# Performance work log

Hardware: AMD Instinct MI355X
Metric: run time of the kernel (lower is better)

The kernel has to match this reference:

```python
import jax, jax.numpy as jnp
import numpy as np

MI, MH, MO = 8, 16, 8  # multiplicities of (0e,1o) in in/hidden/out irreps
NB = 262144

_eps = np.zeros((3, 3, 3), dtype=np.float32)
_eps[0, 1, 2] = _eps[1, 2, 0] = _eps[2, 0, 1] = 1.0
_eps[0, 2, 1] = _eps[2, 1, 0] = _eps[1, 0, 2] = -1.0
EPS_LC = jnp.asarray(_eps)  # Levi-Civita; w3j(1,1,1) = eps/sqrt(6)


def fctp(s, v, w_ss, w_vv0, w_sv, w_vs, w_vv1):
    """FullyConnectedTensorProduct for irreps (ms x 0e + mv x 1o) -> (mw x 0e + mw_v x 1o).
    e3nn 'component' irrep normalization + 'element' path normalization:
    path_weight = sqrt(ir_out.dim / sum_paths(mul1*mul2)).
    w3j(0,0,0)=1, w3j(1,1,0)=delta/sqrt(3), w3j(0,1,1)=delta/sqrt(3), w3j(1,1,1)=eps/sqrt(6)."""
    ms, mv = s.shape[1], v.shape[1]
    c0 = (1.0 / (ms * ms + mv * mv)) ** 0.5          # scalar output: paths ss->s, vv->s
    c1 = (3.0 / (2 * ms * mv + mv * mv)) ** 0.5      # vector output: paths sv, vs, vv
    inv3 = 3.0 ** -0.5
    inv6 = 6.0 ** -0.5
    out_s = c0 * (jnp.einsum('bu,bv,uvw->bw', s, s, w_ss)
                  + inv3 * jnp.einsum('bui,bvi,uvw->bw', v, v, w_vv0))
    out_v = c1 * (inv3 * (jnp.einsum('bu,bvi,uvw->bwi', s, v, w_sv)
                          + jnp.einsum('bui,bv,uvw->bwi', v, s, w_vs))
                  + inv6 * jnp.einsum('bui,bvj,uvw,ijk->bwk', v, v, w_vv1, EPS_LC))
    return out_s, out_v


def si_norm(ys, yv, eps=1e-9):
    """SelfInteraction variance normalization (torch.std is unbiased -> ddof=1)."""
    std_s = jnp.std(ys, axis=1, ddof=1)
    ys = ys / (std_s[:, None] + eps)
    norm1 = jnp.sqrt(jnp.sum(yv ** 2, axis=2) + eps)   # [nb, mv]
    std_v = jnp.std(norm1, axis=1, ddof=1)
    yv = yv / (std_v[:, None, None] + eps)
    return ys, yv


def tv_norm(xs, xv, eps=1e-6):
    xs = xs / jnp.sqrt(jnp.sum(xs ** 2, axis=1, keepdims=True) + eps)
    # faithful to torch: sum over channel dim -> [nb,3], then mean over the 3 comps
    norm1 = jnp.sqrt(jnp.sum(xv ** 2, axis=1) + eps)   # [nb, 3]
    norm_mean = jnp.mean(norm1, axis=1)                # [nb]
    xv = xv / (norm_mean[:, None, None] + eps)
    return xs, xv


def setup_inputs() -> dict:
    key = jax.random.key(0)
    ks = jax.random.split(key, 11)
    x = jax.random.normal(ks[0], (NB, MI + 3 * MI), dtype=jnp.float32)
    # e3nn initializes tensor-product weights ~ N(0,1); normalization via path weights
    w1 = {n: jax.random.normal(k, (MI, MI, MH), dtype=jnp.float32)
          for n, k in zip(['w1_ss', 'w1_vv0', 'w1_sv', 'w1_vs', 'w1_vv1'], ks[1:6])}
    w2 = {n: jax.random.normal(k, (MH, MH, MO), dtype=jnp.float32)
          for n, k in zip(['w2_ss', 'w2_vv0', 'w2_sv', 'w2_vs', 'w2_vv1'], ks[6:11])}
    return {'x': x, **w1, **w2}


def reference(x, w1_ss, w1_vv0, w1_sv, w1_vs, w1_vv1,
              w2_ss, w2_vv0, w2_sv, w2_vs, w2_vv1):
    nb = x.shape[0]
    # layout: [scalars(MI) | vectors(MI*3, u-major)]
    xs = jnp.tanh(x[:, :MI])                    # Activation(tanh) on l=0 only
    xv = x[:, MI:].reshape(nb, MI, 3)
    ys, yv = fctp(xs, xv, w1_ss, w1_vv0, w1_sv, w1_vs, w1_vv1)   # si1 tensor product
    ys, yv = si_norm(ys, yv)                    # si1 variance normalization
    ys, yv = tv_norm(ys, yv)                    # TvNorm
    zs, zv = fctp(ys, yv, w2_ss, w2_vv0, w2_sv, w2_vs, w2_vv1)   # si2 tensor product
    zs, zv = si_norm(zs, zv)
    zs = jax.nn.sigmoid(zs)                     # Activation(sigmoid) on l=0 only
    return jnp.concatenate([zs, zv.reshape(nb, MO * 3)], axis=1)
```

## Files before the change

kernel.cpp:

```cpp
#include <hip/hip_runtime.h>
#include <math.h>

#define NBROWS 262144

typedef float v2f __attribute__((ext_vector_type(2)));
__device__ __forceinline__ v2f sp(float x){ v2f r; r.x = x; r.y = x; return r; }

#define WS_TOT 7808

__device__ void pair_le(int p, int M, int& u, int& v) {
    u = 0; int cnt = M;
    while (p >= cnt) { p -= cnt; ++u; cnt = M - u; }
    v = u + p;
}
__device__ void pair_lt(int p, int M, int& u, int& v) {
    u = 0; int cnt = M - 1;
    while (p >= cnt) { p -= cnt; ++u; cnt = M - 1 - u; }
    v = u + 1 + p;
}

__global__ __launch_bounds__(256) void prep_kernel(
    const float* __restrict__ w1_ss, const float* __restrict__ w1_vv0,
    const float* __restrict__ w1_sv, const float* __restrict__ w1_vs,
    const float* __restrict__ w1_vv1,
    const float* __restrict__ w2_ss, const float* __restrict__ w2_vv0,
    const float* __restrict__ w2_sv, const float* __restrict__ w2_vs,
    const float* __restrict__ w2_vv1,
    float* __restrict__ ws)
{
    const float inv3 = 0.5773502691896258f;
    const float inv6 = 0.4082482904638631f;
    int i = blockIdx.x * 256 + threadIdx.x;
    if (i >= WS_TOT) return;
    float val = 0.f;
    if (i < 1152) {
        int p = i >> 5, r = i & 31;
        int which = r >> 4, w = r & 15;
        int u, v; pair_le(p, 8, u, v);
        const float c0 = 0.08838834764831845f;
        const float* src = which ? w1_vv0 : w1_ss;
        float cc = which ? c0 * inv3 : c0;
        val = (u == v) ? cc * src[(u*8+v)*16+w]
                       : cc * (src[(u*8+v)*16+w] + src[(v*8+u)*16+w]);
    } else if (i < 2176) {
        int r = i - 1152; int vv = r >> 7, rem = r & 127, u = rem >> 4, w = rem & 15;
        val = (0.125f * inv3) * (w1_sv[(u*8+vv)*16+w] + w1_vs[(vv*8+u)*16+w]);
    } else if (i < 2624) {
        int r = i - 2176; int p = r >> 4, w = r & 15;
        int u, v; pair_lt(p, 8, u, v);
        val = (0.125f * inv6) * (w1_vv1[(u*8+v)*16+w] - w1_vv1[(v*8+u)*16+w]);
    } else if (i < 4800) {
        int r = i - 2624; int p = r >> 4, rr = r & 15, which = rr >> 3, w = rr & 7;
        int u, v; pair_le(p, 16, u, v);
        const float c0 = 0.04419417382415922f;
        const float* src = which ? w2_vv0 : w2_ss;
        float cc = which ? c0 * inv3 : c0;
        val = (u == v) ? cc * src[(u*16+v)*8+w]
                       : cc * (src[(u*16+v)*8+w] + src[(v*16+u)*8+w]);
    } else if (i < 6848) {
        int r = i - 4800; int vv = r >> 7, rem = r & 127, u = rem >> 3, w = rem & 7;
        val = (0.0625f * inv3) * (w2_sv[(u*16+vv)*8+w] + w2_vs[(vv*16+u)*8+w]);
    } else {
        int r = i - 6848; int p = r >> 3, w = r & 7;
        int u, v; pair_lt(p, 16, u, v);
        val = (0.0625f * inv6) * (w2_vv1[(u*16+v)*8+w] - w2_vv1[(v*16+u)*8+w]);
    }
    ws[i] = val;
}

template<int W0>
__device__ __forceinline__ void l1_chunk(const float* Wl,
    const float (&s)[8], const float (&v)[8][3],
    v2f (&ys2)[8], v2f (&ox)[8], v2f (&oy)[8], v2f (&oz)[8])
{
    const int J0 = W0 / 2;
#pragma unroll
    for (int j = 0; j < 4; ++j) { ys2[J0+j]=sp(0.f); ox[J0+j]=sp(0.f); oy[J0+j]=sp(0.f); oz[J0+j]=sp(0.f); }
    {
        int p = 0;
#pragma unroll
        for (int u = 0; u < 8; ++u)
#pragma unroll
        for (int vv = u; vv < 8; ++vv) {
            float pp = s[u] * s[vv];
            float dd = v[u][0]*v[vv][0] + v[u][1]*v[vv][1] + v[u][2]*v[vv][2];
            const v2f* qa = reinterpret_cast<const v2f*>(Wl + p*32 + W0);
            const v2f* qb = reinterpret_cast<const v2f*>(Wl + p*32 + 16 + W0);
            v2f vp = sp(pp), vd = sp(dd);
#pragma unroll
            for (int j = 0; j < 4; ++j) ys2[J0+j] += vp*qa[j] + vd*qb[j];
            ++p;
        }
    }
#pragma unroll
    for (int vv = 0; vv < 8; ++vv) {
        v2f tw[4];
#pragma unroll
        for (int j = 0; j < 4; ++j) tw[j] = sp(0.f);
#pragma unroll
        for (int u = 0; u < 8; ++u) {
            const v2f* qc = reinterpret_cast<const v2f*>(Wl + 1152 + (vv*8+u)*16 + W0);
            v2f su = sp(s[u]);
#pragma unroll
            for (int j = 0; j < 4; ++j) tw[j] += su*qc[j];
        }
        v2f vx = sp(v[vv][0]), vy = sp(v[vv][1]), vz = sp(v[vv][2]);
#pragma unroll
        for (int j = 0; j < 4; ++j) {
            ox[J0+j] += tw[j]*vx; oy[J0+j] += tw[j]*vy; oz[J0+j] += tw[j]*vz;
        }
    }
    {
        int p = 0;
#pragma unroll
        for (int u = 0; u < 8; ++u)
#pragma unroll
        for (int vv = u + 1; vv < 8; ++vv) {
            float cx = v[u][1]*v[vv][2] - v[u][2]*v[vv][1];
            float cy = v[u][2]*v[vv][0] - v[u][0]*v[vv][2];
            float cz = v[u][0]*v[vv][1] - v[u][1]*v[vv][0];
            const v2f* qa = reinterpret_cast<const v2f*>(Wl + 2176 + p*16 + W0);
            v2f vcx = sp(cx), vcy = sp(cy), vcz = sp(cz);
#pragma unroll
            for (int j = 0; j < 4; ++j) {
                v2f a = qa[j];
                ox[J0+j] += vcx*a; oy[J0+j] += vcy*a; oz[J0+j] += vcz*a;
            }
            ++p;
        }
    }
}

__device__ __forceinline__ void l2_pass(const float* Wl,
    const float (&s)[16], const float (&v)[16][3],
    v2f (&zs2)[4], v2f (&zx)[4], v2f (&zy)[4], v2f (&zz)[4])
{
#pragma unroll
    for (int j = 0; j < 4; ++j) { zs2[j]=sp(0.f); zx[j]=sp(0.f); zy[j]=sp(0.f); zz[j]=sp(0.f); }
    {
        int p = 0;
#pragma unroll
        for (int u = 0; u < 16; ++u)
#pragma unroll
        for (int vv = u; vv < 16; ++vv) {
            float pp = s[u] * s[vv];
            float dd = v[u][0]*v[vv][0] + v[u][1]*v[vv][1] + v[u][2]*v[vv][2];
            const v2f* qa = reinterpret_cast<const v2f*>(Wl + 2624 + p*16);
            const v2f* qb = reinterpret_cast<const v2f*>(Wl + 2624 + p*16 + 8);
            v2f vp = sp(pp), vd = sp(dd);
#pragma unroll
            for (int j = 0; j < 4; ++j) zs2[j] += vp*qa[j] + vd*qb[j];
            ++p;
        }
    }
#pragma unroll
    for (int vv = 0; vv < 16; ++vv) {
        v2f tw[4];
#pragma unroll
        for (int j = 0; j < 4; ++j) tw[j] = sp(0.f);
#pragma unroll
        for (int u = 0; u < 16; ++u) {
            const v2f* qc = reinterpret_cast<const v2f*>(Wl + 4800 + (vv*16+u)*8);
            v2f su = sp(s[u]);
#pragma unroll
            for (int j = 0; j < 4; ++j) tw[j] += su*qc[j];
        }
        v2f vx = sp(v[vv][0]), vy = sp(v[vv][1]), vz = sp(v[vv][2]);
#pragma unroll
        for (int j = 0; j < 4; ++j) {
            zx[j] += tw[j]*vx; zy[j] += tw[j]*vy; zz[j] += tw[j]*vz;
        }
    }
    {
        int p = 0;
#pragma unroll
        for (int u = 0; u < 16; ++u)
#pragma unroll
        for (int vv = u + 1; vv < 16; ++vv) {
            float cx = v[u][1]*v[vv][2] - v[u][2]*v[vv][1];
            float cy = v[u][2]*v[vv][0] - v[u][0]*v[vv][2];
            float cz = v[u][0]*v[vv][1] - v[u][1]*v[vv][0];
            const v2f* qa = reinterpret_cast<const v2f*>(Wl + 6848 + p*8);
            v2f vcx = sp(cx), vcy = sp(cy), vcz = sp(cz);
#pragma unroll
            for (int j = 0; j < 4; ++j) {
                v2f a = qa[j];
                zx[j] += vcx*a; zy[j] += vcy*a; zz[j] += vcz*a;
            }
            ++p;
        }
    }
}

__device__ __forceinline__ void si_norm16_v(v2f (&ys2)[8], v2f (&ox)[8], v2f (&oy)[8], v2f (&oz)[8])
{
    v2f a = sp(0.f);
#pragma unroll
    for (int j = 0; j < 8; ++j) a += ys2[j];
    float m = (a.x + a.y) * (1.f/16);
    v2f vr = sp(0.f);
#pragma unroll
    for (int j = 0; j < 8; ++j) { v2f d = ys2[j] - sp(m); vr += d*d; }
    float inv = 1.f / (sqrtf((vr.x+vr.y) * (1.f/15)) + 1e-9f);
#pragma unroll
    for (int j = 0; j < 8; ++j) ys2[j] *= sp(inv);

    float n1[16]; float sum = 0.f;
#pragma unroll
    for (int j = 0; j < 8; ++j) {
        v2f nn = ox[j]*ox[j] + oy[j]*oy[j] + oz[j]*oz[j];
        n1[2*j]   = sqrtf(nn.x + 1e-9f);
        n1[2*j+1] = sqrtf(nn.y + 1e-9f);
        sum += n1[2*j] + n1[2*j+1];
    }
    float mn = sum * (1.f/16);
    float var = 0.f;
#pragma unroll
    for (int i = 0; i < 16; ++i) { float d = n1[i] - mn; var += d*d; }
    float invv = 1.f / (sqrtf(var * (1.f/15)) + 1e-9f);
    v2f vi = sp(invv);
#pragma unroll
    for (int j = 0; j < 8; ++j) { ox[j] *= vi; oy[j] *= vi; oz[j] *= vi; }
}

__device__ __forceinline__ void tv_norm16_v(v2f (&ys2)[8], v2f (&ox)[8], v2f (&oy)[8], v2f (&oz)[8])
{
    v2f ssum = sp(0.f);
#pragma unroll
    for (int j = 0; j < 8; ++j) ssum += ys2[j]*ys2[j];
    float inv = 1.f / sqrtf(ssum.x + ssum.y + 1e-6f);
#pragma unroll
    for (int j = 0; j < 8; ++j) ys2[j] *= sp(inv);

    v2f sx = sp(0.f), sy = sp(0.f), sz = sp(0.f);
#pragma unroll
    for (int j = 0; j < 8; ++j) { sx += ox[j]*ox[j]; sy += oy[j]*oy[j]; sz += oz[j]*oz[j]; }
    float nm = (sqrtf(sx.x+sx.y+1e-6f) + sqrtf(sy.x+sy.y+1e-6f) + sqrtf(sz.x+sz.y+1e-6f)) * (1.f/3.f);
    float invv = 1.f / (nm + 1e-6f);
#pragma unroll
    for (int j = 0; j < 8; ++j) { ox[j] *= sp(invv); oy[j] *= sp(invv); oz[j] *= sp(invv); }
}

__device__ __forceinline__ void si_norm8_v(v2f (&zs2)[4], v2f (&zx)[4], v2f (&zy)[4], v2f (&zz)[4])
{
    v2f a = sp(0.f);
#pragma unroll
    for (int j = 0; j < 4; ++j) a += zs2[j];
    float m = (a.x + a.y) * (1.f/8);
    v2f vr = sp(0.f);
#pragma unroll
    for (int j = 0; j < 4; ++j) { v2f d = zs2[j] - sp(m); vr += d*d; }
    float inv = 1.f / (sqrtf((vr.x+vr.y) * (1.f/7)) + 1e-9f);
#pragma unroll
    for (int j = 0; j < 4; ++j) zs2[j] *= sp(inv);

    float n1[8]; float sum = 0.f;
#pragma unroll
    for (int j = 0; j < 4; ++j) {
        v2f nn = zx[j]*zx[j] + zy[j]*zy[j] + zz[j]*zz[j];
        n1[2*j]   = sqrtf(nn.x + 1e-9f);
        n1[2*j+1] = sqrtf(nn.y + 1e-9f);
        sum += n1[2*j] + n1[2*j+1];
    }
    float mn = sum * (1.f/8);
    float var = 0.f;
#pragma unroll
    for (int i = 0; i < 8; ++i) { float d = n1[i] - mn; var += d*d; }
    float invv = 1.f / (sqrtf(var * (1.f/7)) + 1e-9f);
    v2f vi = sp(invv);
#pragma unroll
    for (int j = 0; j < 4; ++j) { zx[j] *= vi; zy[j] *= vi; zz[j] *= vi; }
}

__device__ __forceinline__ float fast_tanh(float x) {
    return 1.f - 2.f / (__expf(2.f * x) + 1.f);
}

__global__ __launch_bounds__(256) void DoubleLayer_main_kernel(
    const float* __restrict__ x,
    const float* __restrict__ ws,
    float* __restrict__ out)
{
    __shared__ float Wl[WS_TOT];

    int row = blockIdx.x * 256 + threadIdx.x;
    const float4* xr = reinterpret_cast<const float4*>(x + (size_t)row * 32);
    float4 q0 = xr[0], q1 = xr[1], q2 = xr[2], q3 = xr[3];
    float4 q4 = xr[4], q5 = xr[5], q6 = xr[6], q7 = xr[7];

#pragma unroll
    for (int i = 0; i < 8; ++i) {
        int idx = threadIdx.x + i * 256;
        if (idx < WS_TOT/4)
            reinterpret_cast<float4*>(Wl)[idx] = reinterpret_cast<const float4*>(ws)[idx];
    }
    __syncthreads();

    float s1[8];
    s1[0] = fast_tanh(q0.x); s1[1] = fast_tanh(q0.y); s1[2] = fast_tanh(q0.z); s1[3] = fast_tanh(q0.w);
    s1[4] = fast_tanh(q1.x); s1[5] = fast_tanh(q1.y); s1[6] = fast_tanh(q1.z); s1[7] = fast_tanh(q1.w);
    float v1[8][3];
    v1[0][0]=q2.x; v1[0][1]=q2.y; v1[0][2]=q2.z;
    v1[1][0]=q2.w; v1[1][1]=q3.x; v1[1][2]=q3.y;
    v1[2][0]=q3.z; v1[2][1]=q3.w; v1[2][2]=q4.x;
    v1[3][0]=q4.y; v1[3][1]=q4.z; v1[3][2]=q4.w;
    v1[4][0]=q5.x; v1[4][1]=q5.y; v1[4][2]=q5.z;
    v1[5][0]=q5.w; v1[5][1]=q6.x; v1[5][2]=q6.y;
    v1[6][0]=q6.z; v1[6][1]=q6.w; v1[6][2]=q7.x;
    v1[7][0]=q7.y; v1[7][1]=q7.z; v1[7][2]=q7.w;

    v2f ys2[8], ox[8], oy[8], oz[8];
    l1_chunk<0>(Wl, s1, v1, ys2, ox, oy, oz);
    __builtin_amdgcn_sched_barrier(0);
    l1_chunk<8>(Wl, s1, v1, ys2, ox, oy, oz);
    __builtin_amdgcn_sched_barrier(0);

    si_norm16_v(ys2, ox, oy, oz);
    tv_norm16_v(ys2, ox, oy, oz);
    __builtin_amdgcn_sched_barrier(0);

    float s2[16], vv2[16][3];
#pragma unroll
    for (int j = 0; j < 8; ++j) {
        s2[2*j] = ys2[j].x;   s2[2*j+1] = ys2[j].y;
        vv2[2*j][0] = ox[j].x; vv2[2*j+1][0] = ox[j].y;
        vv2[2*j][1] = oy[j].x; vv2[2*j+1][1] = oy[j].y;
        vv2[2*j][2] = oz[j].x; vv2[2*j+1][2] = oz[j].y;
    }

    v2f zs2[4], zx[4], zy[4], zz[4];
    l2_pass(Wl, s2, vv2, zs2, zx, zy, zz);
    __builtin_amdgcn_sched_barrier(0);

    si_norm8_v(zs2, zx, zy, zz);

    float o[32];
#pragma unroll
    for (int j = 0; j < 4; ++j) {
        o[2*j]   = 1.f / (1.f + __expf(-zs2[j].x));
        o[2*j+1] = 1.f / (1.f + __expf(-zs2[j].y));
    }
#pragma unroll
    for (int j = 0; j < 4; ++j) {
        int w0 = 2*j, w1 = 2*j+1;
        o[8+3*w0+0] = zx[j].x; o[8+3*w0+1] = zy[j].x; o[8+3*w0+2] = zz[j].x;
        o[8+3*w1+0] = zx[j].y; o[8+3*w1+1] = zy[j].y; o[8+3*w1+2] = zz[j].y;
    }
    float4* orow = reinterpret_cast<float4*>(out + (size_t)row * 32);
#pragma unroll
    for (int i = 0; i < 8; ++i) orow[i] = make_float4(o[4*i+0], o[4*i+1], o[4*i+2], o[4*i+3]);
}

extern "C" void kernel_launch(void* const* d_in, const int* in_sizes, int n_in,
                              void* d_out, int out_size, void* d_ws, size_t ws_size,
                              hipStream_t stream)
{
    const float* x = (const float*)d_in[0];
    float* ws = (float*)d_ws;
    prep_kernel<<<31, 256, 0, stream>>>(
        (const float*)d_in[1], (const float*)d_in[2], (const float*)d_in[3],
        (const float*)d_in[4], (const float*)d_in[5],
        (const float*)d_in[6], (const float*)d_in[7], (const float*)d_in[8],
        (const float*)d_in[9], (const float*)d_in[10], ws);
    DoubleLayer_main_kernel<<<NBROWS/256, 256, 0, stream>>>(x, ws, (float*)d_out);
}
```

Measured before the change: 202.9 us.

## Process two rows per thread packed into v2f lanes with inline pk_fma

Each thread now handles two rows, one per half of each packed float2, instead of packing two output channels of a single row. Inline-asm v_pk_fma_f32 with op_sel broadcasts individual weight lanes, so the per-pair products (s*s, dot, cross) are computed once for both rows and each LDS weight load is shared by two rows. The norm routines are rewritten to work per lane. The intent is to halve the per-pair scalar work and LDS traffic per row. In exchange, register pressure roughly doubles (accumulators for 16 channels times two rows) and the grid is halved, which may lower occupancy or cause spills.

```diff
diff --git a/kernel.cpp b/kernel.cpp
--- a/kernel.cpp
+++ b/kernel.cpp
@@ -4,7 +4,26 @@
 #define NBROWS 262144
 
 typedef float v2f __attribute__((ext_vector_type(2)));
-__device__ __forceinline__ v2f sp(float x){ v2f r; r.x = x; r.y = x; return r; }
+__device__ __forceinline__ v2f pkset(float a, float b){ v2f r; r.x=a; r.y=b; return r; }
+__device__ __forceinline__ v2f sp(float a){ return pkset(a,a); }
+
+__device__ __forceinline__ void fma2(v2f& d, v2f a, v2f b){
+    asm("v_pk_fma_f32 %0, %1, %2, %0" : "+v"(d) : "v"(a), "v"(b));
+}
+__device__ __forceinline__ void fma2n(v2f& d, v2f a, v2f b){
+    asm("v_pk_fma_f32 %0, %1, %2, %0 neg_lo:[1,0,0] neg_hi:[1,0,0]" : "+v"(d) : "v"(a), "v"(b));
+}
+__device__ __forceinline__ void fma2_lo(v2f& d, v2f a, v2f w){
+    asm("v_pk_fma_f32 %0, %1, %2, %0 op_sel_hi:[1,0,1]" : "+v"(d) : "v"(a), "v"(w));
+}
+__device__ __forceinline__ void fma2_hi(v2f& d, v2f a, v2f w){
+    asm("v_pk_fma_f32 %0, %1, %2, %0 op_sel:[0,1,0] op_sel_hi:[1,1,1]" : "+v"(d) : "v"(a), "v"(w));
+}
+__device__ __forceinline__ v2f mul2(v2f a, v2f b){
+    v2f d; asm("v_pk_mul_f32 %0, %1, %2" : "=v"(d) : "v"(a), "v"(b)); return d;
+}
+__device__ __forceinline__ v2f sqrt2(v2f a){ return pkset(sqrtf(a.x), sqrtf(a.y)); }
+__device__ __forceinline__ v2f rcp2(v2f a){ return pkset(1.f/a.x, 1.f/a.y); }
 
 #define WS_TOT 7808
 
@@ -70,44 +89,49 @@
 
 template<int W0>
 __device__ __forceinline__ void l1_chunk(const float* Wl,
-    const float (&s)[8], const float (&v)[8][3],
-    v2f (&ys2)[8], v2f (&ox)[8], v2f (&oy)[8], v2f (&oz)[8])
-{
-    const int J0 = W0 / 2;
-#pragma unroll
-    for (int j = 0; j < 4; ++j) { ys2[J0+j]=sp(0.f); ox[J0+j]=sp(0.f); oy[J0+j]=sp(0.f); oz[J0+j]=sp(0.f); }
+    const v2f (&s)[8], const v2f (&vx1)[8], const v2f (&vy1)[8], const v2f (&vz1)[8],
+    v2f (&ys)[16], v2f (&vx)[16], v2f (&vy)[16], v2f (&vz)[16])
+{
+#pragma unroll
+    for (int w = 0; w < 8; ++w) { ys[W0+w]=sp(0.f); vx[W0+w]=sp(0.f); vy[W0+w]=sp(0.f); vz[W0+w]=sp(0.f); }
     {
         int p = 0;
 #pragma unroll
         for (int u = 0; u < 8; ++u)
 #pragma unroll
         for (int vv = u; vv < 8; ++vv) {
-            float pp = s[u] * s[vv];
-            float dd = v[u][0]*v[vv][0] + v[u][1]*v[vv][1] + v[u][2]*v[vv][2];
+            v2f pp = mul2(s[u], s[vv]);
+            v2f dd = mul2(vx1[u], vx1[vv]); fma2(dd, vy1[u], vy1[vv]); fma2(dd, vz1[u], vz1[vv]);
             const v2f* qa = reinterpret_cast<const v2f*>(Wl + p*32 + W0);
             const v2f* qb = reinterpret_cast<const v2f*>(Wl + p*32 + 16 + W0);
-            v2f vp = sp(pp), vd = sp(dd);
-#pragma unroll
-            for (int j = 0; j < 4; ++j) ys2[J0+j] += vp*qa[j] + vd*qb[j];
+#pragma unroll
+            for (int j = 0; j < 4; ++j) {
+                v2f wa = qa[j], wb = qb[j];
+                fma2_lo(ys[W0+2*j],   pp, wa); fma2_hi(ys[W0+2*j+1], pp, wa);
+                fma2_lo(ys[W0+2*j],   dd, wb); fma2_hi(ys[W0+2*j+1], dd, wb);
+            }
             ++p;
         }
     }
 #pragma unroll
     for (int vv = 0; vv < 8; ++vv) {
-        v2f tw[4];
-#pragma unroll
-        for (int j = 0; j < 4; ++j) tw[j] = sp(0.f);
+        v2f tw[8];
+#pragma unroll
+        for (int w = 0; w < 8; ++w) tw[w] = sp(0.f);
 #pragma unroll
         for (int u = 0; u < 8; ++u) {
             const v2f* qc = reinterpret_cast<const v2f*>(Wl + 1152 + (vv*8+u)*16 + W0);
-            v2f su = sp(s[u]);
-#pragma unroll
-            for (int j = 0; j < 4; ++j) tw[j] += su*qc[j];
-        }
-        v2f vx = sp(v[vv][0]), vy = sp(v[vv][1]), vz = sp(v[vv][2]);
-#pragma unroll
-        for (int j = 0; j < 4; ++j) {
-            ox[J0+j] += tw[j]*vx; oy[J0+j] += tw[j]*vy; oz[J0+j] += tw[j]*vz;
+#pragma unroll
+            for (int j = 0; j < 4; ++j) {
+                v2f wc = qc[j];
+                fma2_lo(tw[2*j], s[u], wc); fma2_hi(tw[2*j+1], s[u], wc);
+            }
+        }
+#pragma unroll
+        for (int w = 0; w < 8; ++w) {
+            fma2(vx[W0+w], tw[w], vx1[vv]);
+            fma2(vy[W0+w], tw[w], vy1[vv]);
+            fma2(vz[W0+w], tw[w], vz1[vv]);
         }
     }
     {
@@ -116,40 +140,45 @@
         for (int u = 0; u < 8; ++u)
 #pragma unroll
         for (int vv = u + 1; vv < 8; ++vv) {
-            float cx = v[u][1]*v[vv][2] - v[u][2]*v[vv][1];
-            float cy = v[u][2]*v[vv][0] - v[u][0]*v[vv][2];
-            float cz = v[u][0]*v[vv][1] - v[u][1]*v[vv][0];
+            v2f cx = mul2(vy1[u], vz1[vv]); fma2n(cx, vz1[u], vy1[vv]);
+            v2f cy = mul2(vz1[u], vx1[vv]); fma2n(cy, vx1[u], vz1[vv]);
+            v2f cz = mul2(vx1[u], vy1[vv]); fma2n(cz, vy1[u], vx1[vv]);
             const v2f* qa = reinterpret_cast<const v2f*>(Wl + 2176 + p*16 + W0);
-            v2f vcx = sp(cx), vcy = sp(cy), vcz = sp(cz);
 #pragma unroll
             for (int j = 0; j < 4; ++j) {
-                v2f a = qa[j];
-                ox[J0+j] += vcx*a; oy[J0+j] += vcy*a; oz[J0+j] += vcz*a;
+                v2f wa = qa[j];
+                fma2_lo(vx[W0+2*j], cx, wa); fma2_hi(vx[W0+2*j+1], cx, wa);
+                fma2_lo(vy[W0+2*j], cy, wa); fma2_hi(vy[W0+2*j+1], cy, wa);
+                fma2_lo(vz[W0+2*j], cz, wa); fma2_hi(vz[W0+2*j+1], cz, wa);
             }
             ++p;
         }
     }
 }
 
-__device__ __forceinline__ void l2_pass(const float* Wl,
-    const float (&s)[16], const float (&v)[16][3],
-    v2f (&zs2)[4], v2f (&zx)[4], v2f (&zy)[4], v2f (&zz)[4])
-{
-#pragma unroll
-    for (int j = 0; j < 4; ++j) { zs2[j]=sp(0.f); zx[j]=sp(0.f); zy[j]=sp(0.f); zz[j]=sp(0.f); }
+template<int W0>
+__device__ __forceinline__ void l2_chunk(const float* Wl,
+    const v2f (&s)[16], const v2f (&vx1)[16], const v2f (&vy1)[16], const v2f (&vz1)[16],
+    v2f (&zs)[8], v2f (&zx)[8], v2f (&zy)[8], v2f (&zz)[8])
+{
+#pragma unroll
+    for (int w = 0; w < 4; ++w) { zs[W0+w]=sp(0.f); zx[W0+w]=sp(0.f); zy[W0+w]=sp(0.f); zz[W0+w]=sp(0.f); }
     {
         int p = 0;
 #pragma unroll
         for (int u = 0; u < 16; ++u)
 #pragma unroll
         for (int vv = u; vv < 16; ++vv) {
-            float pp = s[u] * s[vv];
-            float dd = v[u][0]*v[vv][0] + v[u][1]*v[vv][1] + v[u][2]*v[vv][2];
-            const v2f* qa = reinterpret_cast<const v2f*>(Wl + 2624 + p*16);
-            const v2f* qb = reinterpret_cast<const v2f*>(Wl + 2624 + p*16 + 8);
-            v2f vp = sp(pp), vd = sp(dd);
-#pragma unroll
-            for (int j = 0; j < 4; ++j) zs2[j] += vp*qa[j] + vd*qb[j];
+            v2f pp = mul2(s[u], s[vv]);
+            v2f dd = mul2(vx1[u], vx1[vv]); fma2(dd, vy1[u], vy1[vv]); fma2(dd, vz1[u], vz1[vv]);
+            const v2f* qa = reinterpret_cast<const v2f*>(Wl + 2624 + p*16 + W0);
+            const v2f* qb = reinterpret_cast<const v2f*>(Wl + 2624 + p*16 + 8 + W0);
+#pragma unroll
+            for (int j = 0; j < 2; ++j) {
+                v2f wa = qa[j], wb = qb[j];
+                fma2_lo(zs[W0+2*j],   pp, wa); fma2_hi(zs[W0+2*j+1], pp, wa);
+                fma2_lo(zs[W0+2*j],   dd, wb); fma2_hi(zs[W0+2*j+1], dd, wb);
+            }
             ++p;
         }
     }
@@ -157,18 +186,21 @@
     for (int vv = 0; vv < 16; ++vv) {
         v2f tw[4];
 #pragma unroll
-        for (int j = 0; j < 4; ++j) tw[j] = sp(0.f);
+        for (int w = 0; w < 4; ++w) tw[w] = sp(0.f);
 #pragma unroll
         for (int u = 0; u < 16; ++u) {
-            const v2f* qc = reinterpret_cast<const v2f*>(Wl + 4800 + (vv*16+u)*8);
-            v2f su = sp(s[u]);
-#pragma unroll
-            for (int j = 0; j < 4; ++j) tw[j] += su*qc[j];
-        }
-        v2f vx = sp(v[vv][0]), vy = sp(v[vv][1]), vz = sp(v[vv][2]);
-#pragma unroll
-        for (int j = 0; j < 4; ++j) {
-            zx[j] += tw[j]*vx; zy[j] += tw[j]*vy; zz[j] += tw[j]*vz;
+            const v2f* qc = reinterpret_cast<const v2f*>(Wl + 4800 + (vv*16+u)*8 + W0);
+#pragma unroll
+            for (int j = 0; j < 2; ++j) {
+                v2f wc = qc[j];
+                fma2_lo(tw[2*j], s[u], wc); fma2_hi(tw[2*j+1], s[u], wc);
+            }
+        }
+#pragma unroll
+        for (int w = 0; w < 4; ++w) {
+            fma2(zx[W0+w], tw[w], vx1[vv]);
+            fma2(zy[W0+w], tw[w], vy1[vv]);
+            fma2(zz[W0+w], tw[w], vz1[vv]);
         }
     }
     {
@@ -177,99 +209,96 @@
         for (int u = 0; u < 16; ++u)
 #pragma unroll
         for (int vv = u + 1; vv < 16; ++vv) {
-            float cx = v[u][1]*v[vv][2] - v[u][2]*v[vv][1];
-            float cy = v[u][2]*v[vv][0] - v[u][0]*v[vv][2];
-            float cz = v[u][0]*v[vv][1] - v[u][1]*v[vv][0];
-            const v2f* qa = reinterpret_cast<const v2f*>(Wl + 6848 + p*8);
-            v2f vcx = sp(cx), vcy = sp(cy), vcz = sp(cz);
-#pragma unroll
-            for (int j = 0; j < 4; ++j) {
-                v2f a = qa[j];
-                zx[j] += vcx*a; zy[j] += vcy*a; zz[j] += vcz*a;
+            v2f cx = mul2(vy1[u], vz1[vv]); fma2n(cx, vz1[u], vy1[vv]);
+            v2f cy = mul2(vz1[u], vx1[vv]); fma2n(cy, vx1[u], vz1[vv]);
+            v2f cz = mul2(vx1[u], vy1[vv]); fma2n(cz, vy1[u], vx1[vv]);
+            const v2f* qa = reinterpret_cast<const v2f*>(Wl + 6848 + p*8 + W0);
+#pragma unroll
+            for (int j = 0; j < 2; ++j) {
+                v2f wa = qa[j];
+                fma2_lo(zx[W0+2*j], cx, wa); fma2_hi(zx[W0+2*j+1], cx, wa);
+                fma2_lo(zy[W0+2*j], cy, wa); fma2_hi(zy[W0+2*j+1], cy, wa);
+                fma2_lo(zz[W0+2*j], cz, wa); fma2_hi(zz[W0+2*j+1], cz, wa);
             }
             ++p;
         }
     }
 }
 
-__device__ __forceinline__ void si_norm16_v(v2f (&ys2)[8], v2f (&ox)[8], v2f (&oy)[8], v2f (&oz)[8])
+__device__ __forceinline__ void si_norm16_p(v2f (&ys)[16], v2f (&vx)[16], v2f (&vy)[16], v2f (&vz)[16])
 {
     v2f a = sp(0.f);
 #pragma unroll
-    for (int j = 0; j < 8; ++j) a += ys2[j];
-    float m = (a.x + a.y) * (1.f/16);
+    for (int j = 0; j < 16; ++j) a += ys[j];
+    v2f m = a * sp(1.f/16);
+    v2f var = sp(0.f);
+#pragma unroll
+    for (int j = 0; j < 16; ++j) { v2f d = ys[j] - m; fma2(var, d, d); }
+    v2f inv = rcp2(sqrt2(var * sp(1.f/15)) + sp(1e-9f));
+#pragma unroll
+    for (int j = 0; j < 16; ++j) ys[j] = mul2(ys[j], inv);
+
+    v2f n[16]; v2f sn = sp(0.f);
+#pragma unroll
+    for (int j = 0; j < 16; ++j) {
+        v2f nn = mul2(vx[j], vx[j]); fma2(nn, vy[j], vy[j]); fma2(nn, vz[j], vz[j]);
+        n[j] = sqrt2(nn + sp(1e-9f));
+        sn += n[j];
+    }
+    v2f mn = sn * sp(1.f/16);
     v2f vr = sp(0.f);
 #pragma unroll
-    for (int j = 0; j < 8; ++j) { v2f d = ys2[j] - sp(m); vr += d*d; }
-    float inv = 1.f / (sqrtf((vr.x+vr.y) * (1.f/15)) + 1e-9f);
-#pragma unroll
-    for (int j = 0; j < 8; ++j) ys2[j] *= sp(inv);
-
-    float n1[16]; float sum = 0.f;
+    for (int j = 0; j < 16; ++j) { v2f d = n[j] - mn; fma2(vr, d, d); }
+    v2f invv = rcp2(sqrt2(vr * sp(1.f/15)) + sp(1e-9f));
+#pragma unroll
+    for (int j = 0; j < 16; ++j) { vx[j]=mul2(vx[j],invv); vy[j]=mul2(vy[j],invv); vz[j]=mul2(vz[j],invv); }
+}
+
+__device__ __forceinline__ void tv_norm16_p(v2f (&ys)[16], v2f (&vx)[16], v2f (&vy)[16], v2f (&vz)[16])
+{
+    v2f ss = sp(0.f);
+#pragma unroll
+    for (int j = 0; j < 16; ++j) fma2(ss, ys[j], ys[j]);
+    v2f inv = rcp2(sqrt2(ss + sp(1e-6f)));
+#pragma unroll
+    for (int j = 0; j < 16; ++j) ys[j] = mul2(ys[j], inv);
+
+    v2f sx = sp(0.f), sy = sp(0.f), sz = sp(0.f);
+#pragma unroll
+    for (int j = 0; j < 16; ++j) { fma2(sx, vx[j], vx[j]); fma2(sy, vy[j], vy[j]); fma2(sz, vz[j], vz[j]); }
+    v2f nm = (sqrt2(sx + sp(1e-6f)) + sqrt2(sy + sp(1e-6f)) + sqrt2(sz + sp(1e-6f))) * sp(1.f/3.f);
+    v2f invv = rcp2(nm + sp(1e-6f));
+#pragma unroll
+    for (int j = 0; j < 16; ++j) { vx[j]=mul2(vx[j],invv); vy[j]=mul2(vy[j],invv); vz[j]=mul2(vz[j],invv); }
+}
+
+__device__ __forceinline__ void si_norm8_p(v2f (&zs)[8], v2f (&zx)[8], v2f (&zy)[8], v2f (&zz)[8])
+{
+    v2f a = sp(0.f);
+#pragma unroll
+    for (int j = 0; j < 8; ++j) a += zs[j];
+    v2f m = a * sp(1.f/8);
+    v2f var = sp(0.f);
+#pragma unroll
+    for (int j = 0; j < 8; ++j) { v2f d = zs[j] - m; fma2(var, d, d); }
+    v2f inv = rcp2(sqrt2(var * sp(1.f/7)) + sp(1e-9f));
+#pragma unroll
+    for (int j = 0; j < 8; ++j) zs[j] = mul2(zs[j], inv);
+
+    v2f n[8]; v2f sn = sp(0.f);
 #pragma unroll
     for (int j = 0; j < 8; ++j) {
-        v2f nn = ox[j]*ox[j] + oy[j]*oy[j] + oz[j]*oz[j];
-        n1[2*j]   = sqrtf(nn.x + 1e-9f);
-        n1[2*j+1] = sqrtf(nn.y + 1e-9f);
-        sum += n1[2*j] + n1[2*j+1];
-    }
-    float mn = sum * (1.f/16);
-    float var = 0.f;
-#pragma unroll
-    for (int i = 0; i < 16; ++i) { float d = n1[i] - mn; var += d*d; }
-    float invv = 1.f / (sqrtf(var * (1.f/15)) + 1e-9f);
-    v2f vi = sp(invv);
-#pragma unroll
-    for (int j = 0; j < 8; ++j) { ox[j] *= vi; oy[j] *= vi; oz[j] *= vi; }
-}
-
-__device__ __forceinline__ void tv_norm16_v(v2f (&ys2)[8], v2f (&ox)[8], v2f (&oy)[8], v2f (&oz)[8])
-{
-    v2f ssum = sp(0.f);
-#pragma unroll
-    for (int j = 0; j < 8; ++j) ssum += ys2[j]*ys2[j];
-    float inv = 1.f / sqrtf(ssum.x + ssum.y + 1e-6f);
-#pragma unroll
-    for (int j = 0; j < 8; ++j) ys2[j] *= sp(inv);
-
-    v2f sx = sp(0.f), sy = sp(0.f), sz = sp(0.f);
-#pragma unroll
-    for (int j = 0; j < 8; ++j) { sx += ox[j]*ox[j]; sy += oy[j]*oy[j]; sz += oz[j]*oz[j]; }
-    float nm = (sqrtf(sx.x+sx.y+1e-6f) + sqrtf(sy.x+sy.y+1e-6f) + sqrtf(sz.x+sz.y+1e-6f)) * (1.f/3.f);
-    float invv = 1.f / (nm + 1e-6f);
-#pragma unroll
-    for (int j = 0; j < 8; ++j) { ox[j] *= sp(invv); oy[j] *= sp(invv); oz[j] *= sp(invv); }
-}
-
-__device__ __forceinline__ void si_norm8_v(v2f (&zs2)[4], v2f (&zx)[4], v2f (&zy)[4], v2f (&zz)[4])
-{
-    v2f a = sp(0.f);
-#pragma unroll
-    for (int j = 0; j < 4; ++j) a += zs2[j];
-    float m = (a.x + a.y) * (1.f/8);
+        v2f nn = mul2(zx[j], zx[j]); fma2(nn, zy[j], zy[j]); fma2(nn, zz[j], zz[j]);
+        n[j] = sqrt2(nn + sp(1e-9f));
+        sn += n[j];
+    }
+    v2f mn = sn * sp(1.f/8);
     v2f vr = sp(0.f);
 #pragma unroll
-    for (int j = 0; j < 4; ++j) { v2f d = zs2[j] - sp(m); vr += d*d; }
-    float inv = 1.f / (sqrtf((vr.x+vr.y) * (1.f/7)) + 1e-9f);
-#pragma unroll
-    for (int j = 0; j < 4; ++j) zs2[j] *= sp(inv);
-
-    float n1[8]; float sum = 0.f;
-#pragma unroll
-    for (int j = 0; j < 4; ++j) {
-        v2f nn = zx[j]*zx[j] + zy[j]*zy[j] + zz[j]*zz[j];
-        n1[2*j]   = sqrtf(nn.x + 1e-9f);
-        n1[2*j+1] = sqrtf(nn.y + 1e-9f);
-        sum += n1[2*j] + n1[2*j+1];
-    }
-    float mn = sum * (1.f/8);
-    float var = 0.f;
-#pragma unroll
-    for (int i = 0; i < 8; ++i) { float d = n1[i] - mn; var += d*d; }
-    float invv = 1.f / (sqrtf(var * (1.f/7)) + 1e-9f);
-    v2f vi = sp(invv);
-#pragma unroll
-    for (int j = 0; j < 4; ++j) { zx[j] *= vi; zy[j] *= vi; zz[j] *= vi; }
+    for (int j = 0; j < 8; ++j) { v2f d = n[j] - mn; fma2(vr, d, d); }
+    v2f invv = rcp2(sqrt2(vr * sp(1.f/7)) + sp(1e-9f));
+#pragma unroll
+    for (int j = 0; j < 8; ++j) { zx[j]=mul2(zx[j],invv); zy[j]=mul2(zy[j],invv); zz[j]=mul2(zz[j],invv); }
 }
 
 __device__ __forceinline__ float fast_tanh(float x) {
@@ -283,72 +312,78 @@
 {
     __shared__ float Wl[WS_TOT];
 
-    int row = blockIdx.x * 256 + threadIdx.x;
-    const float4* xr = reinterpret_cast<const float4*>(x + (size_t)row * 32);
-    float4 q0 = xr[0], q1 = xr[1], q2 = xr[2], q3 = xr[3];
-    float4 q4 = xr[4], q5 = xr[5], q6 = xr[6], q7 = xr[7];
+    int t = threadIdx.x;
+    int rA = blockIdx.x * 512 + t;
+    int rB = rA + 256;
+    const float4* xa = reinterpret_cast<const float4*>(x + (size_t)rA * 32);
+    const float4* xb = reinterpret_cast<const float4*>(x + (size_t)rB * 32);
+    float4 a0 = xa[0], a1 = xa[1], a2 = xa[2], a3 = xa[3];
+    float4 a4 = xa[4], a5 = xa[5], a6 = xa[6], a7 = xa[7];
+    float4 b0 = xb[0], b1 = xb[1], b2 = xb[2], b3 = xb[3];
+    float4 b4 = xb[4], b5 = xb[5], b6 = xb[6], b7 = xb[7];
 
 #pragma unroll
     for (int i = 0; i < 8; ++i) {
-        int idx = threadIdx.x + i * 256;
+        int idx = t + i * 256;
         if (idx < WS_TOT/4)
             reinterpret_cast<float4*>(Wl)[idx] = reinterpret_cast<const float4*>(ws)[idx];
     }
     __syncthreads();
 
-    float s1[8];
-    s1[0] = fast_tanh(q0.x); s1[1] = fast_tanh(q0.y); s1[2] = fast_tanh(q0.z); s1[3] = fast_tanh(q0.w);
-    s1[4] = fast_tanh(q1.x); s1[5] = fast_tanh(q1.y); s1[6] = fast_tanh(q1.z); s1[7] = fast_tanh(q1.w);
-    float v1[8][3];
-    v1[0][0]=q2.x; v1[0][1]=q2.y; v1[0][2]=q2.z;
-    v1[1][0]=q2.w; v1[1][1]=q3.x; v1[1][2]=q3.y;
-    v1[2][0]=q3.z; v1[2][1]=q3.w; v1[2][2]=q4.x;
-    v1[3][0]=q4.y; v1[3][1]=q4.z; v1[3][2]=q4.w;
-    v1[4][0]=q5.x; v1[4][1]=q5.y; v1[4][2]=q5.z;
-    v1[5][0]=q5.w; v1[5][1]=q6.x; v1[5][2]=q6.y;
-    v1[6][0]=q6.z; v1[6][1]=q6.w; v1[6][2]=q7.x;
-    v1[7][0]=q7.y; v1[7][1]=q7.z; v1[7][2]=q7.w;
-
-    v2f ys2[8], ox[8], oy[8], oz[8];
-    l1_chunk<0>(Wl, s1, v1, ys2, ox, oy, oz);
+    v2f s1[8], v1x[8], v1y[8], v1z[8];
+    s1[0] = pkset(fast_tanh(a0.x), fast_tanh(b0.x));
+    s1[1] = pkset(fast_tanh(a0.y), fast_tanh(b0.y));
+    s1[2] = pkset(fast_tanh(a0.z), fast_tanh(b0.z));
+    s1[3] = pkset(fast_tanh(a0.w), fast_tanh(b0.w));
+    s1[4] = pkset(fast_tanh(a1.x), fast_tanh(b1.x));
+    s1[5] = pkset(fast_tanh(a1.y), fast_tanh(b1.y));
+    s1[6] = pkset(fast_tanh(a1.z), fast_tanh(b1.z));
+    s1[7] = pkset(fast_tanh(a1.w), fast_tanh(b1.w));
+    v1x[0]=pkset(a2.x,b2.x); v1y[0]=pkset(a2.y,b2.y); v1z[0]=pkset(a2.z,b2.z);
+    v1x[1]=pkset(a2.w,b2.w); v1y[1]=pkset(a3.x,b3.x); v1z[1]=pkset(a3.y,b3.y);
+    v1x[2]=pkset(a3.z,b3.z); v1y[2]=pkset(a3.w,b3.w); v1z[2]=pkset(a4.x,b4.x);
+    v1x[3]=pkset(a4.y,b4.y); v1y[3]=pkset(a4.z,b4.z); v1z[3]=pkset(a4.w,b4.w);
+    v1x[4]=pkset(a5.x,b5.x); v1y[4]=pkset(a5.y,b5.y); v1z[4]=pkset(a5.z,b5.z);
+    v1x[5]=pkset(a5.w,b5.w); v1y[5]=pkset(a6.x,b6.x); v1z[5]=pkset(a6.y,b6.y);
+    v1x[6]=pkset(a6.z,b6.z); v1y[6]=pkset(a6.w,b6.w); v1z[6]=pkset(a7.x,b7.x);
+    v1x[7]=pkset(a7.y,b7.y); v1y[7]=pkset(a7.z,b7.z); v1z[7]=pkset(a7.w,b7.w);
+
+    v2f ys[16], vx[16], vy[16], vz[16];
+    l1_chunk<0>(Wl, s1, v1x, v1y, v1z, ys, vx, vy, vz);
     __builtin_amdgcn_sched_barrier(0);
-    l1_chunk<8>(Wl, s1, v1, ys2, ox, oy, oz);
+    l1_chunk<8>(Wl, s1, v1x, v1y, v1z, ys, vx, vy, vz);
     __builtin_amdgcn_sched_barrier(0);
 
-    si_norm16_v(ys2, ox, oy, oz);
-    tv_norm16_v(ys2, ox, oy, oz);
+    si_norm16_p(ys, vx, vy, vz);
+    tv_norm16_p(ys, vx, vy, vz);
     __builtin_amdgcn_sched_barrier(0);
 
-    float s2[16], vv2[16][3];
-#pragma unroll
-    for (int j = 0; j < 8; ++j) {
-        s2[2*j] = ys2[j].x;   s2[2*j+1] = ys2[j].y;
-        vv2[2*j][0] = ox[j].x; vv2[2*j+1][0] = ox[j].y;
-        vv2[2*j][1] = oy[j].x; vv2[2*j+1][1] = oy[j].y;
-        vv2[2*j][2] = oz[j].x; vv2[2*j+1][2] = oz[j].y;
-    }
-
-    v2f zs2[4], zx[4], zy[4], zz[4];
-    l2_pass(Wl, s2, vv2, zs2, zx, zy, zz);
+    v2f zs[8], zx[8], zy[8], zz[8];
+    l2_chunk<0>(Wl, ys, vx, vy, vz, zs, zx, zy, zz);
     __builtin_amdgcn_sched_barrier(0);
-
-    si_norm8_v(zs2, zx, zy, zz);
-
-    float o[32];
-#pragma unroll
-    for (int j = 0; j < 4; ++j) {
-        o[2*j]   = 1.f / (1.f + __expf(-zs2[j].x));
-        o[2*j+1] = 1.f / (1.f + __expf(-zs2[j].y));
-    }
-#pragma unroll
-    for (int j = 0; j < 4; ++j) {
-        int w0 = 2*j, w1 = 2*j+1;
-        o[8+3*w0+0] = zx[j].x; o[8+3*w0+1] = zy[j].x; o[8+3*w0+2] = zz[j].x;
-        o[8+3*w1+0] = zx[j].y; o[8+3*w1+1] = zy[j].y; o[8+3*w1+2] = zz[j].y;
-    }
-    float4* orow = reinterpret_cast<float4*>(out + (size_t)row * 32);
-#pragma unroll
-    for (int i = 0; i < 8; ++i) orow[i] = make_float4(o[4*i+0], o[4*i+1], o[4*i+2], o[4*i+3]);
+    l2_chunk<4>(Wl, ys, vx, vy, vz, zs, zx, zy, zz);
+    __builtin_amdgcn_sched_barrier(0);
+
+    si_norm8_p(zs, zx, zy, zz);
+
+    float oA[32], oB[32];
+#pragma unroll
+    for (int w = 0; w < 8; ++w) {
+        oA[w] = 1.f / (1.f + __expf(-zs[w].x));
+        oB[w] = 1.f / (1.f + __expf(-zs[w].y));
+    }
+#pragma unroll
+    for (int w = 0; w < 8; ++w) {
+        oA[8+3*w+0] = zx[w].x; oA[8+3*w+1] = zy[w].x; oA[8+3*w+2] = zz[w].x;
+        oB[8+3*w+0] = zx[w].y; oB[8+3*w+1] = zy[w].y; oB[8+3*w+2] = zz[w].y;
+    }
+    float4* oa = reinterpret_cast<float4*>(out + (size_t)rA * 32);
+    float4* ob = reinterpret_cast<float4*>(out + (size_t)rB * 32);
+#pragma unroll
+    for (int i = 0; i < 8; ++i) {
+        oa[i] = make_float4(oA[4*i+0], oA[4*i+1], oA[4*i+2], oA[4*i+3]);
+        ob[i] = make_float4(oB[4*i+0], oB[4*i+1], oB[4*i+2], oB[4*i+3]);
+    }
 }
 
 extern "C" void kernel_launch(void* const* d_in, const int* in_sizes, int n_in,
@@ -362,5 +397,5 @@
         (const float*)d_in[4], (const float*)d_in[5],
         (const float*)d_in[6], (const float*)d_in[7], (const float*)d_in[8],
         (const float*)d_in[9], (const float*)d_in[10], ws);
-    DoubleLayer_main_kernel<<<NBROWS/256, 256, 0, stream>>>(x, ws, (float*)d_out);
-}
+    DoubleLayer_main_kernel<<<NBROWS/512, 256, 0, stream>>>(x, ws, (float*)d_out);
+}
```

After: 674.6 us. +232.5%, slower.

## Split fused kernel into two layer kernels with fp16 intermediate in output buffer

Applied to the files above, without the earlier changes.

Splits the single fused kernel into a layer-1 kernel and a layer-2 kernel. The normalized hidden features are written as packed fp16 into the output buffer and read back by the second kernel, which overwrites the same rows in place. Each kernel keeps only its own weights in shared memory and has a smaller register footprint, which should allow higher occupancy. The cost is an extra round-trip through global memory and an added launch, and storing the hidden state in fp16 reduces precision.

```diff
diff --git a/kernel.cpp b/kernel.cpp
--- a/kernel.cpp
+++ b/kernel.cpp
@@ -1,10 +1,21 @@
 #include <hip/hip_runtime.h>
+#include <hip/hip_fp16.h>
 #include <math.h>
 
 #define NBROWS 262144
 
 typedef float v2f __attribute__((ext_vector_type(2)));
-__device__ __forceinline__ v2f sp(float x){ v2f r; r.x = x; r.y = x; return r; }
+__device__ __forceinline__ v2f pkset(float a, float b){ v2f r; r.x=a; r.y=b; return r; }
+__device__ __forceinline__ v2f sp(float a){ return pkset(a,a); }
+
+__device__ __forceinline__ unsigned pack_h2(v2f a){
+    __half2 h = __floats2half2_rn(a.x, a.y);
+    unsigned u; __builtin_memcpy(&u, &h, 4); return u;
+}
+__device__ __forceinline__ float2 unpack_h2(unsigned u){
+    __half2 h; __builtin_memcpy(&h, &u, 4);
+    return __half22float2(h);
+}
 
 #define WS_TOT 7808
 
@@ -71,11 +82,11 @@
 template<int W0>
 __device__ __forceinline__ void l1_chunk(const float* Wl,
     const float (&s)[8], const float (&v)[8][3],
-    v2f (&ys2)[8], v2f (&ox)[8], v2f (&oy)[8], v2f (&oz)[8])
+    v2f (&ys)[8], v2f (&ox)[8], v2f (&oy)[8], v2f (&oz)[8])
 {
     const int J0 = W0 / 2;
 #pragma unroll
-    for (int j = 0; j < 4; ++j) { ys2[J0+j]=sp(0.f); ox[J0+j]=sp(0.f); oy[J0+j]=sp(0.f); oz[J0+j]=sp(0.f); }
+    for (int j = 0; j < 4; ++j) { ys[J0+j]=sp(0.f); ox[J0+j]=sp(0.f); oy[J0+j]=sp(0.f); oz[J0+j]=sp(0.f); }
     {
         int p = 0;
 #pragma unroll
@@ -88,7 +99,7 @@
             const v2f* qb = reinterpret_cast<const v2f*>(Wl + p*32 + 16 + W0);
             v2f vp = sp(pp), vd = sp(dd);
 #pragma unroll
-            for (int j = 0; j < 4; ++j) ys2[J0+j] += vp*qa[j] + vd*qb[j];
+            for (int j = 0; j < 4; ++j) ys[J0+j] += vp*qa[j] + vd*qb[j];
             ++p;
         }
     }
@@ -133,10 +144,10 @@
 
 __device__ __forceinline__ void l2_pass(const float* Wl,
     const float (&s)[16], const float (&v)[16][3],
-    v2f (&zs2)[4], v2f (&zx)[4], v2f (&zy)[4], v2f (&zz)[4])
-{
-#pragma unroll
-    for (int j = 0; j < 4; ++j) { zs2[j]=sp(0.f); zx[j]=sp(0.f); zy[j]=sp(0.f); zz[j]=sp(0.f); }
+    v2f (&zs)[4], v2f (&zx)[4], v2f (&zy)[4], v2f (&zz)[4])
+{
+#pragma unroll
+    for (int j = 0; j < 4; ++j) { zs[j]=sp(0.f); zx[j]=sp(0.f); zy[j]=sp(0.f); zz[j]=sp(0.f); }
     {
         int p = 0;
 #pragma unroll
@@ -145,11 +156,11 @@
         for (int vv = u; vv < 16; ++vv) {
             float pp = s[u] * s[vv];
             float dd = v[u][0]*v[vv][0] + v[u][1]*v[vv][1] + v[u][2]*v[vv][2];
-            const v2f* qa = reinterpret_cast<const v2f*>(Wl + 2624 + p*16);
-            const v2f* qb = reinterpret_cast<const v2f*>(Wl + 2624 + p*16 + 8);
+            const v2f* qa = reinterpret_cast<const v2f*>(Wl + p*16);
+            const v2f* qb = reinterpret_cast<const v2f*>(Wl + p*16 + 8);
             v2f vp = sp(pp), vd = sp(dd);
 #pragma unroll
-            for (int j = 0; j < 4; ++j) zs2[j] += vp*qa[j] + vd*qb[j];
+            for (int j = 0; j < 4; ++j) zs[j] += vp*qa[j] + vd*qb[j];
             ++p;
         }
     }
@@ -160,7 +171,7 @@
         for (int j = 0; j < 4; ++j) tw[j] = sp(0.f);
 #pragma unroll
         for (int u = 0; u < 16; ++u) {
-            const v2f* qc = reinterpret_cast<const v2f*>(Wl + 4800 + (vv*16+u)*8);
+            const v2f* qc = reinterpret_cast<const v2f*>(Wl + 2176 + (vv*16+u)*8);
             v2f su = sp(s[u]);
 #pragma unroll
             for (int j = 0; j < 4; ++j) tw[j] += su*qc[j];
@@ -180,7 +191,7 @@
             float cx = v[u][1]*v[vv][2] - v[u][2]*v[vv][1];
             float cy = v[u][2]*v[vv][0] - v[u][0]*v[vv][2];
             float cz = v[u][0]*v[vv][1] - v[u][1]*v[vv][0];
-            const v2f* qa = reinterpret_cast<const v2f*>(Wl + 6848 + p*8);
+            const v2f* qa = reinterpret_cast<const v2f*>(Wl + 4224 + p*8);
             v2f vcx = sp(cx), vcy = sp(cy), vcz = sp(cz);
 #pragma unroll
             for (int j = 0; j < 4; ++j) {
@@ -192,18 +203,18 @@
     }
 }
 
-__device__ __forceinline__ void si_norm16_v(v2f (&ys2)[8], v2f (&ox)[8], v2f (&oy)[8], v2f (&oz)[8])
+__device__ __forceinline__ void si_norm16_v(v2f (&ys)[8], v2f (&ox)[8], v2f (&oy)[8], v2f (&oz)[8])
 {
     v2f a = sp(0.f);
 #pragma unroll
-    for (int j = 0; j < 8; ++j) a += ys2[j];
+    for (int j = 0; j < 8; ++j) a += ys[j];
     float m = (a.x + a.y) * (1.f/16);
     v2f vr = sp(0.f);
 #pragma unroll
-    for (int j = 0; j < 8; ++j) { v2f d = ys2[j] - sp(m); vr += d*d; }
+    for (int j = 0; j < 8; ++j) { v2f d = ys[j] - sp(m); vr += d*d; }
     float inv = 1.f / (sqrtf((vr.x+vr.y) * (1.f/15)) + 1e-9f);
 #pragma unroll
-    for (int j = 0; j < 8; ++j) ys2[j] *= sp(inv);
+    for (int j = 0; j < 8; ++j) ys[j] *= sp(inv);
 
     float n1[16]; float sum = 0.f;
 #pragma unroll
@@ -223,14 +234,14 @@
     for (int j = 0; j < 8; ++j) { ox[j] *= vi; oy[j] *= vi; oz[j] *= vi; }
 }
 
-__device__ __forceinline__ void tv_norm16_v(v2f (&ys2)[8], v2f (&ox)[8], v2f (&oy)[8], v2f (&oz)[8])
+__device__ __forceinline__ void tv_norm16_v(v2f (&ys)[8], v2f (&ox)[8], v2f (&oy)[8], v2f (&oz)[8])
 {
     v2f ssum = sp(0.f);
 #pragma unroll
-    for (int j = 0; j < 8; ++j) ssum += ys2[j]*ys2[j];
+    for (int j = 0; j < 8; ++j) ssum += ys[j]*ys[j];
     float inv = 1.f / sqrtf(ssum.x + ssum.y + 1e-6f);
 #pragma unroll
-    for (int j = 0; j < 8; ++j) ys2[j] *= sp(inv);
+    for (int j = 0; j < 8; ++j) ys[j] *= sp(inv);
 
     v2f sx = sp(0.f), sy = sp(0.f), sz = sp(0.f);
 #pragma unroll
@@ -241,18 +252,18 @@
     for (int j = 0; j < 8; ++j) { ox[j] *= sp(invv); oy[j] *= sp(invv); oz[j] *= sp(invv); }
 }
 
-__device__ __forceinline__ void si_norm8_v(v2f (&zs2)[4], v2f (&zx)[4], v2f (&zy)[4], v2f (&zz)[4])
+__device__ __forceinline__ void si_norm8_v(v2f (&zs)[4], v2f (&zx)[4], v2f (&zy)[4], v2f (&zz)[4])
 {
     v2f a = sp(0.f);
 #pragma unroll
-    for (int j = 0; j < 4; ++j) a += zs2[j];
+    for (int j = 0; j < 4; ++j) a += zs[j];
     float m = (a.x + a.y) * (1.f/8);
     v2f vr = sp(0.f);
 #pragma unroll
-    for (int j = 0; j < 4; ++j) { v2f d = zs2[j] - sp(m); vr += d*d; }
+    for (int j = 0; j < 4; ++j) { v2f d = zs[j] - sp(m); vr += d*d; }
     float inv = 1.f / (sqrtf((vr.x+vr.y) * (1.f/7)) + 1e-9f);
 #pragma unroll
-    for (int j = 0; j < 4; ++j) zs2[j] *= sp(inv);
+    for (int j = 0; j < 4; ++j) zs[j] *= sp(inv);
 
     float n1[8]; float sum = 0.f;
 #pragma unroll
@@ -276,22 +287,23 @@
     return 1.f - 2.f / (__expf(2.f * x) + 1.f);
 }
 
-__global__ __launch_bounds__(256) void DoubleLayer_main_kernel(
+__global__ __launch_bounds__(256) void DoubleLayer_l1_kernel(
     const float* __restrict__ x,
     const float* __restrict__ ws,
-    float* __restrict__ out)
-{
-    __shared__ float Wl[WS_TOT];
-
-    int row = blockIdx.x * 256 + threadIdx.x;
+    unsigned* __restrict__ inter)
+{
+    __shared__ float Wl[2624];
+
+    int t = threadIdx.x;
+    int row = blockIdx.x * 256 + t;
     const float4* xr = reinterpret_cast<const float4*>(x + (size_t)row * 32);
     float4 q0 = xr[0], q1 = xr[1], q2 = xr[2], q3 = xr[3];
     float4 q4 = xr[4], q5 = xr[5], q6 = xr[6], q7 = xr[7];
 
 #pragma unroll
-    for (int i = 0; i < 8; ++i) {
-        int idx = threadIdx.x + i * 256;
-        if (idx < WS_TOT/4)
+    for (int i = 0; i < 3; ++i) {
+        int idx = t + i * 256;
+        if (idx < 656)
             reinterpret_cast<float4*>(Wl)[idx] = reinterpret_cast<const float4*>(ws)[idx];
     }
     __syncthreads();
@@ -309,36 +321,79 @@
     v1[6][0]=q6.z; v1[6][1]=q6.w; v1[6][2]=q7.x;
     v1[7][0]=q7.y; v1[7][1]=q7.z; v1[7][2]=q7.w;
 
-    v2f ys2[8], ox[8], oy[8], oz[8];
-    l1_chunk<0>(Wl, s1, v1, ys2, ox, oy, oz);
+    v2f ys[8], ox[8], oy[8], oz[8];
+    l1_chunk<0>(Wl, s1, v1, ys, ox, oy, oz);
     __builtin_amdgcn_sched_barrier(0);
-    l1_chunk<8>(Wl, s1, v1, ys2, ox, oy, oz);
+    l1_chunk<8>(Wl, s1, v1, ys, ox, oy, oz);
     __builtin_amdgcn_sched_barrier(0);
 
-    si_norm16_v(ys2, ox, oy, oz);
-    tv_norm16_v(ys2, ox, oy, oz);
+    si_norm16_v(ys, ox, oy, oz);
+    tv_norm16_v(ys, ox, oy, oz);
+
+    unsigned* orow = inter + (size_t)row * 32;
+    uint4* o4 = reinterpret_cast<uint4*>(orow);
+#pragma unroll
+    for (int j = 0; j < 2; ++j)
+        o4[j] = make_uint4(pack_h2(ys[4*j]), pack_h2(ys[4*j+1]), pack_h2(ys[4*j+2]), pack_h2(ys[4*j+3]));
+#pragma unroll
+    for (int j = 0; j < 2; ++j)
+        o4[2+j] = make_uint4(pack_h2(ox[4*j]), pack_h2(ox[4*j+1]), pack_h2(ox[4*j+2]), pack_h2(ox[4*j+3]));
+#pragma unroll
+    for (int j = 0; j < 2; ++j)
+        o4[4+j] = make_uint4(pack_h2(oy[4*j]), pack_h2(oy[4*j+1]), pack_h2(oy[4*j+2]), pack_h2(oy[4*j+3]));
+#pragma unroll
+    for (int j = 0; j < 2; ++j)
+        o4[6+j] = make_uint4(pack_h2(oz[4*j]), pack_h2(oz[4*j+1]), pack_h2(oz[4*j+2]), pack_h2(oz[4*j+3]));
+}
+
+__global__ __launch_bounds__(256) void DoubleLayer_l2_kernel(
+    const float* __restrict__ ws,
+    float* __restrict__ out)
+{
+    __shared__ float Wl[5184];
+
+    int t = threadIdx.x;
+    int row = blockIdx.x * 256 + t;
+    const uint4* irow = reinterpret_cast<const uint4*>(out + (size_t)row * 32);
+    uint4 h0 = irow[0], h1 = irow[1], h2 = irow[2], h3 = irow[3];
+    uint4 h4 = irow[4], h5 = irow[5], h6 = irow[6], h7 = irow[7];
+
+    const float4* wsrc = reinterpret_cast<const float4*>(ws + 2624);
+#pragma unroll
+    for (int i = 0; i < 6; ++i) {
+        int idx = t + i * 256;
+        if (idx < 1296)
+            reinterpret_cast<float4*>(Wl)[idx] = wsrc[idx];
+    }
+    __syncthreads();
+
+    float s2[16], vv2[16][3];
+    {
+        unsigned us[8] = {h0.x,h0.y,h0.z,h0.w,h1.x,h1.y,h1.z,h1.w};
+        unsigned ux[8] = {h2.x,h2.y,h2.z,h2.w,h3.x,h3.y,h3.z,h3.w};
+        unsigned uy[8] = {h4.x,h4.y,h4.z,h4.w,h5.x,h5.y,h5.z,h5.w};
+        unsigned uz[8] = {h6.x,h6.y,h6.z,h6.w,h7.x,h7.y,h7.z,h7.w};
+#pragma unroll
+        for (int j = 0; j < 8; ++j) {
+            float2 fs = unpack_h2(us[j]); s2[2*j] = fs.x; s2[2*j+1] = fs.y;
+            float2 fx = unpack_h2(ux[j]); vv2[2*j][0] = fx.x; vv2[2*j+1][0] = fx.y;
+            float2 fy = unpack_h2(uy[j]); vv2[2*j][1] = fy.x; vv2[2*j+1][1] = fy.y;
+            float2 fz = unpack_h2(uz[j]); vv2[2*j][2] = fz.x; vv2[2*j+1][2] = fz.y;
+        }
+    }
     __builtin_amdgcn_sched_barrier(0);
 
-    float s2[16], vv2[16][3];
-#pragma unroll
-    for (int j = 0; j < 8; ++j) {
-        s2[2*j] = ys2[j].x;   s2[2*j+1] = ys2[j].y;
-        vv2[2*j][0] = ox[j].x; vv2[2*j+1][0] = ox[j].y;
-        vv2[2*j][1] = oy[j].x; vv2[2*j+1][1] = oy[j].y;
-        vv2[2*j][2] = oz[j].x; vv2[2*j+1][2] = oz[j].y;
-    }
-
-    v2f zs2[4], zx[4], zy[4], zz[4];
-    l2_pass(Wl, s2, vv2, zs2, zx, zy, zz);
+    v2f zs[4], zx[4], zy[4], zz[4];
+    l2_pass(Wl, s2, vv2, zs, zx, zy, zz);
     __builtin_amdgcn_sched_barrier(0);
 
-    si_norm8_v(zs2, zx, zy, zz);
+    si_norm8_v(zs, zx, zy, zz);
 
     float o[32];
 #pragma unroll
     for (int j = 0; j < 4; ++j) {
-        o[2*j]   = 1.f / (1.f + __expf(-zs2[j].x));
-        o[2*j+1] = 1.f / (1.f + __expf(-zs2[j].y));
+        o[2*j]   = 1.f / (1.f + __expf(-zs[j].x));
+        o[2*j+1] = 1.f / (1.f + __expf(-zs[j].y));
     }
 #pragma unroll
     for (int j = 0; j < 4; ++j) {
@@ -362,5 +417,6 @@
         (const float*)d_in[4], (const float*)d_in[5],
         (const float*)d_in[6], (const float*)d_in[7], (const float*)d_in[8],
         (const float*)d_in[9], (const float*)d_in[10], ws);
-    DoubleLayer_main_kernel<<<NBROWS/256, 256, 0, stream>>>(x, ws, (float*)d_out);
-}
+    DoubleLayer_l1_kernel<<<NBROWS/256, 256, 0, stream>>>(x, ws, (unsigned*)d_out);
+    DoubleLayer_l2_kernel<<<NBROWS/256, 256, 0, stream>>>(ws, (float*)d_out);
+}
```

Measured after the change: 222.0 us. +9.4%, slower.
